# Performance work log

Measured on AMD Instinct MI355X. Metric: run time of the kernel, lower is better.

## Reference

```python
import jax, jax.numpy as jnp
import numpy as np

B, S, D = 2, 2048, 2048
NH, NKV = 32, 8
HD = D // NH           # 64
GS = NH // NKV         # 4
ROPE_BASE = 10000.0


def _rope_tables(seq_len, head_dim, base):
    inv_freq = 1.0 / (base ** (jnp.arange(head_dim // 2, dtype=jnp.float32) / (head_dim // 2)))
    angles = jnp.arange(seq_len, dtype=jnp.float32)[:, None] * inv_freq[None, :]  # [S, HD/2]
    angles = jnp.concatenate([angles, angles], axis=-1)                            # [S, HD]
    return jnp.cos(angles), jnp.sin(angles)


def _apply_rope(x, cos, sin):
    # x: [B, H, S, HD]
    hd = x.shape[-1]
    x1, x2 = x[..., : hd // 2], x[..., hd // 2 :]
    rotated = jnp.concatenate([-x2, x1], axis=-1)
    return (x * cos[None, None] + rotated * sin[None, None]).astype(x.dtype)


def setup_inputs() -> dict:
    key = jax.random.key(0)
    ks = jax.random.split(key, 5)
    scale = 0.02
    return {
        "x": jax.random.normal(ks[0], (B, S, D), dtype=jnp.float32),
        "Wq": jax.random.normal(ks[1], (D, D), dtype=jnp.float32) * scale,
        "Wk": jax.random.normal(ks[2], (D, NKV * HD), dtype=jnp.float32) * scale,
        "Wv": jax.random.normal(ks[3], (D, NKV * HD), dtype=jnp.float32) * scale,
        "Wo": jax.random.normal(ks[4], (D, D), dtype=jnp.float32) * scale,
    }


def reference(x, Wq, Wk, Wv, Wo):
    b, n, _ = x.shape
    cos, sin = _rope_tables(n, HD, ROPE_BASE)

    q = (x @ Wq).reshape(b, n, NH, HD).transpose(0, 2, 1, 3)    # [B, NH, S, HD]
    k = (x @ Wk).reshape(b, n, NKV, HD).transpose(0, 2, 1, 3)   # [B, NKV, S, HD]
    v = (x @ Wv).reshape(b, n, NKV, HD).transpose(0, 2, 1, 3)

    q = _apply_rope(q, cos, sin)
    k = _apply_rope(k, cos, sin)

    # GQA head sharing: repeat_interleave KV groups to full head count
    k = jnp.repeat(k, GS, axis=1)   # [B, NH, S, HD]
    v = jnp.repeat(v, GS, axis=1)

    scores = jnp.einsum("bhqd,bhkd->bhqk", q, k)                # [B, NH, S, S]
    causal = jnp.triu(jnp.ones((n, n), dtype=bool), k=1)
    scores = jnp.where(causal[None, None], -jnp.inf, scores)
    weights = jax.nn.softmax(scores / jnp.sqrt(jnp.float32(HD)), axis=-1)

    ctx = jnp.einsum("bhqk,bhkd->bhqd", weights, v)             # [B, NH, S, HD]
    ctx = ctx.transpose(0, 2, 1, 3).reshape(b, n, D)
    return ctx @ Wo
```

## Files before the change

### kernel.cpp

```cpp
#include <hip/hip_runtime.h>

typedef __bf16 bf16;
typedef __attribute__((ext_vector_type(8))) __bf16 bf16x8;
typedef __attribute__((ext_vector_type(4))) float f32x4;
typedef __attribute__((ext_vector_type(4))) short s16x4;

#define S_LEN 2048
#define D_MODEL 2048
#define NHEADS 32
#define NKVH 8
#define HDIM 64
#define BATCH 2

__device__ __forceinline__ void async_cp16(const bf16* g, bf16* l) {
    __builtin_amdgcn_global_load_lds(
        (const __attribute__((address_space(1))) unsigned int*)g,
        (__attribute__((address_space(3))) unsigned int*)l, 16, 0, 0);
}

__global__ void cvt_f32_bf16(const float* __restrict__ in, bf16* __restrict__ out, int n4) {
    int i = blockIdx.x * blockDim.x + threadIdx.x;
    if (i < n4) {
        float4 f = ((const float4*)in)[i];
        union { bf16 h[4]; uint2 u; } t;
        t.h[0] = (bf16)f.x; t.h[1] = (bf16)f.y; t.h[2] = (bf16)f.z; t.h[3] = (bf16)f.w;
        ((uint2*)out)[i] = t.u;
    }
}

__global__ void transpose_w(const float* __restrict__ W, bf16* __restrict__ Wt, int K, int N) {
    __shared__ float tile[32][33];
    int kt = blockIdx.y * 32, nt = blockIdx.x * 32;
    int tx = threadIdx.x, ty = threadIdx.y;
    #pragma unroll
    for (int i = 0; i < 32; i += 8)
        tile[ty + i][tx] = W[(size_t)(kt + ty + i) * N + nt + tx];
    __syncthreads();
    #pragma unroll
    for (int i = 0; i < 32; i += 8)
        Wt[(size_t)(nt + ty + i) * K + kt + tx] = (bf16)tile[tx][ty + i];
}

__global__ void transpose_v(const bf16* __restrict__ QKV, bf16* __restrict__ Vt) {
    __shared__ bf16 tl[32][33];
    int z = blockIdx.z;
    int s0 = blockIdx.x * 32, d0 = blockIdx.y * 32;
    int bb = z >> 3, hh = z & 7;
    int tx = threadIdx.x, ty = threadIdx.y;
    #pragma unroll
    for (int i = 0; i < 32; i += 8)
        tl[ty + i][tx] = QKV[((size_t)(bb * S_LEN + s0 + ty + i)) * 3072 + 2560 + hh * 64 + d0 + tx];
    __syncthreads();
    #pragma unroll
    for (int i = 0; i < 32; i += 8)
        Vt[((size_t)z * 64 + d0 + ty + i) * S_LEN + s0 + tx] = tl[tx][ty + i];
}

template <bool OUT_BF16>
__global__ __launch_bounds__(256) void gemm_bt(const bf16* __restrict__ A,
                                               const bf16* __restrict__ Bt,
                                               void* __restrict__ Cv,
                                               int M, int N, int K) {
    __shared__ __align__(16) bf16 As[128 * 64];
    __shared__ __align__(16) bf16 Bs[128 * 64];

    const int tid  = threadIdx.x;
    const int wave = tid >> 6;
    const int lane = tid & 63;
    const int l16  = lane & 15;
    const int quad = lane >> 4;
    const int wrow = (wave >> 1) * 64;
    const int wcol = (wave & 1) * 64;
    const int m0 = blockIdx.y * 128;
    const int n0 = blockIdx.x * 128;

    const int krow = lane >> 3;
    const int kc   = (lane & 7) ^ krow;
    const bf16* gA = A  + (size_t)(m0 + wave * 32 + krow) * K + kc * 8;
    const bf16* gB = Bt + (size_t)(n0 + wave * 32 + krow) * K + kc * 8;
    bf16* lA = &As[wave * 2048];
    bf16* lB = &Bs[wave * 2048];
    const size_t rstep = (size_t)8 * K;

    const int sw = l16 & 7;

    f32x4 acc[4][4];
    #pragma unroll
    for (int mi = 0; mi < 4; ++mi)
        #pragma unroll
        for (int ni = 0; ni < 4; ++ni)
            acc[mi][ni] = (f32x4){0.f, 0.f, 0.f, 0.f};

    for (int k0 = 0; k0 < K; k0 += 64) {
        __syncthreads();
        async_cp16(gA,             lA);
        async_cp16(gA +     rstep, lA + 512);
        async_cp16(gA + 2 * rstep, lA + 1024);
        async_cp16(gA + 3 * rstep, lA + 1536);
        async_cp16(gB,             lB);
        async_cp16(gB +     rstep, lB + 512);
        async_cp16(gB + 2 * rstep, lB + 1024);
        async_cp16(gB + 3 * rstep, lB + 1536);
        gA += 64; gB += 64;
        __syncthreads();

        #pragma unroll
        for (int kk = 0; kk < 2; ++kk) {
            bf16x8 af[4], bfr[4];
            #pragma unroll
            for (int mi = 0; mi < 4; ++mi)
                af[mi] = *(const bf16x8*)&As[(wrow + mi * 16 + l16) * 64 + (((kk * 4 + quad) ^ sw) * 8)];
            #pragma unroll
            for (int ni = 0; ni < 4; ++ni)
                bfr[ni] = *(const bf16x8*)&Bs[(wcol + ni * 16 + l16) * 64 + (((kk * 4 + quad) ^ sw) * 8)];
            #pragma unroll
            for (int mi = 0; mi < 4; ++mi)
                #pragma unroll
                for (int ni = 0; ni < 4; ++ni)
                    acc[mi][ni] = __builtin_amdgcn_mfma_f32_16x16x32_bf16(af[mi], bfr[ni], acc[mi][ni], 0, 0, 0);
        }
    }

    #pragma unroll
    for (int mi = 0; mi < 4; ++mi) {
        #pragma unroll
        for (int ni = 0; ni < 4; ++ni) {
            #pragma unroll
            for (int r = 0; r < 4; ++r) {
                size_t row = (size_t)(m0 + wrow + mi * 16 + quad * 4 + r);
                size_t col = (size_t)(n0 + wcol + ni * 16 + l16);
                if (OUT_BF16) ((bf16*)Cv)[row * N + col] = (bf16)acc[mi][ni][r];
                else          ((float*)Cv)[row * N + col] = acc[mi][ni][r];
            }
        }
    }
}

__global__ void rope_relayout(const bf16* __restrict__ QKV,
                              bf16* __restrict__ Qr, bf16* __restrict__ Kr) {
    const int QN = BATCH * S_LEN * NHEADS * 32;
    const int KN = BATCH * S_LEN * NKVH * 32;
    const float LC = 0.28782313662425572f;
    int idx = blockIdx.x * 256 + threadIdx.x;
    if (idx < QN) {
        int j = idx & 31, hh = (idx >> 5) & 31, s = (idx >> 10) & 2047, bb = idx >> 21;
        size_t src = ((size_t)(bb * S_LEN + s)) * 3072 + hh * HDIM + j;
        float x1 = (float)QKV[src], x2 = (float)QKV[src + 32];
        float ang = (float)s * __expf(-(float)j * LC);
        float sn, cs; sincosf(ang, &sn, &cs);
        size_t dst = ((size_t)((bb * NHEADS + hh) * S_LEN + s)) * HDIM + j;
        Qr[dst]      = (bf16)((x1 * cs - x2 * sn) * 0.125f);
        Qr[dst + 32] = (bf16)((x2 * cs + x1 * sn) * 0.125f);
    } else if (idx < QN + KN) {
        int t = idx - QN;
        int j = t & 31, hh = (t >> 5) & 7, s = (t >> 8) & 2047, bb = t >> 19;
        size_t src = ((size_t)(bb * S_LEN + s)) * 3072 + 2048 + hh * HDIM + j;
        float x1 = (float)QKV[src], x2 = (float)QKV[src + 32];
        float ang = (float)s * __expf(-(float)j * LC);
        float sn, cs; sincosf(ang, &sn, &cs);
        size_t dst = ((size_t)((bb * NKVH + hh) * S_LEN + s)) * HDIM + j;
        Kr[dst]      = (bf16)(x1 * cs - x2 * sn);
        Kr[dst + 32] = (bf16)(x2 * cs + x1 * sn);
    }
}

__global__ __launch_bounds__(256, 3) void attn_kernel(const bf16* __restrict__ Q,
                                                      const bf16* __restrict__ K,
                                                      const bf16* __restrict__ Vt,
                                                      bf16* __restrict__ Ctx) {
    __shared__ __align__(16) bf16 KsL[128 * 64];
    __shared__ __align__(16) bf16 VtL[64 * 128];

    static const signed char QTAB[16] = {15,14,13,12, 10,11,8,9, 5,4,7,6, 0,1,2,3};
    const int bx = blockIdx.x;
    const int qt = QTAB[((bx >> 8) << 2) | ((bx >> 6) & 3)];
    const int bh = bx & 63;
    const int b  = bh >> 5;
    const int h  = bh & 31;
    const int kvh = h >> 2;
    const int tid = threadIdx.x;
    const int wave = tid >> 6;
    const int lane = tid & 63;
    const int l16  = lane & 15;
    const int quad = lane >> 4;

    const bf16* Qb = Q  + ((size_t)(b * NHEADS + h)) * S_LEN * HDIM;
    const bf16* Kb = K  + ((size_t)(b * NKVH + kvh)) * S_LEN * HDIM;
    const bf16* Vb = Vt + ((size_t)(b * NKVH + kvh)) * HDIM * S_LEN;

    const int q0 = qt * 128;

    bf16x8 aq[2][2];
    #pragma unroll
    for (int qf = 0; qf < 2; ++qf)
        #pragma unroll
        for (int ks = 0; ks < 2; ++ks)
            aq[qf][ks] = *(const bf16x8*)(Qb + (size_t)(q0 + wave * 32 + qf * 16 + l16) * HDIM + ks * 32 + quad * 8);

    f32x4 O[2][4];
    float M0 = -1e30f, M1 = -1e30f;
    float l0 = 0.f, l1 = 0.f;
    #pragma unroll
    for (int qf = 0; qf < 2; ++qf)
        #pragma unroll
        for (int df = 0; df < 4; ++df) O[qf][df] = (f32x4){0.f,0.f,0.f,0.f};

    const int krow = lane >> 3, kslot = lane & 7;
    const int kc   = kslot ^ (krow & 7);
    const int vslot = lane & 15, vsub = lane >> 4;

    #pragma unroll 1
    for (int kt = 0; kt <= qt; ++kt) {
        const int k0 = kt * 128;
        __syncthreads();
        #pragma unroll
        for (int j = 0; j < 4; ++j) {
            int rbase = (wave * 4 + j) * 8;
            async_cp16(Kb + (size_t)(k0 + rbase + krow) * HDIM + kc * 8, &KsL[rbase * 64]);
            int d0 = (wave * 4 + j) * 4;
            int vrow = d0 + vsub;
            int vc = vslot ^ (vrow & 15);
            async_cp16(Vb + (size_t)vrow * S_LEN + k0 + vc * 8, &VtL[d0 * 128]);
        }
        __syncthreads();

        f32x4 sc[2][8];
        #pragma unroll
        for (int kf = 0; kf < 8; ++kf) {
            sc[0][kf] = (f32x4){0.f,0.f,0.f,0.f};
            sc[1][kf] = (f32x4){0.f,0.f,0.f,0.f};
            #pragma unroll
            for (int ks = 0; ks < 2; ++ks) {
                bf16x8 bk = *(const bf16x8*)&KsL[(kf * 16 + l16) * 64 + (((ks * 4 + quad) ^ (l16 & 7)) * 8)];
                sc[0][kf] = __builtin_amdgcn_mfma_f32_16x16x32_bf16(bk, aq[0][ks], sc[0][kf], 0, 0, 0);
                sc[1][kf] = __builtin_amdgcn_mfma_f32_16x16x32_bf16(bk, aq[1][ks], sc[1][kf], 0, 0, 0);
            }
        }

        if (kt == qt) {
            #pragma unroll
            for (int kf = 0; kf < 8; ++kf)
                #pragma unroll
                for (int r = 0; r < 4; ++r) {
                    int key = kf * 16 + quad * 4 + r;
                    int qi0 = wave * 32 + l16;
                    if (key > qi0)      sc[0][kf][r] = -1e30f;
                    if (key > qi0 + 16) sc[1][kf][r] = -1e30f;
                }
        }

        float mx0 = sc[0][0][0], mx1 = sc[1][0][0];
        #pragma unroll
        for (int kf = 0; kf < 8; ++kf)
            #pragma unroll
            for (int r = 0; r < 4; ++r) {
                mx0 = fmaxf(mx0, sc[0][kf][r]);
                mx1 = fmaxf(mx1, sc[1][kf][r]);
            }
        mx0 = fmaxf(mx0, __shfl_xor(mx0, 16)); mx0 = fmaxf(mx0, __shfl_xor(mx0, 32));
        mx1 = fmaxf(mx1, __shfl_xor(mx1, 16)); mx1 = fmaxf(mx1, __shfl_xor(mx1, 32));

        float Mn0 = fmaxf(M0, mx0), Mn1 = fmaxf(M1, mx1);
        float a0 = __expf(M0 - Mn0), a1 = __expf(M1 - Mn1);
        M0 = Mn0; M1 = Mn1;
        l0 *= a0; l1 *= a1;

        #pragma unroll
        for (int r = 0; r < 4; ++r) {
            float aO0 = __shfl(a0, quad * 4 + r);
            float aO1 = __shfl(a1, quad * 4 + r);
            #pragma unroll
            for (int df = 0; df < 4; ++df) {
                O[0][df][r] *= aO0;
                O[1][df][r] *= aO1;
            }
        }

        #pragma unroll
        for (int kf = 0; kf < 8; ++kf)
            #pragma unroll
            for (int r = 0; r < 4; ++r) {
                float e0 = __expf(sc[0][kf][r] - M0); sc[0][kf][r] = e0; l0 += e0;
                float e1 = __expf(sc[1][kf][r] - M1); sc[1][kf][r] = e1; l1 += e1;
            }

        #pragma unroll
        for (int kf = 0; kf < 8; ++kf) {
            union { bf16 hh[4]; s16x4 s4; } p0, p1;
            #pragma unroll
            for (int r = 0; r < 4; ++r) {
                p0.hh[r] = (bf16)sc[0][kf][r];
                p1.hh[r] = (bf16)sc[1][kf][r];
            }
            #pragma unroll
            for (int df = 0; df < 4; ++df) {
                s16x4 bv = *(const s16x4*)&VtL[(df * 16 + l16) * 128 +
                                               (((kf * 2 + (quad >> 1)) ^ l16) * 8) + (quad & 1) * 4];
                O[0][df] = __builtin_amdgcn_mfma_f32_16x16x16bf16_1k(p0.s4, bv, O[0][df], 0, 0, 0);
                O[1][df] = __builtin_amdgcn_mfma_f32_16x16x16bf16_1k(p1.s4, bv, O[1][df], 0, 0, 0);
            }
        }
    }

    l0 += __shfl_xor(l0, 16); l0 += __shfl_xor(l0, 32);
    l1 += __shfl_xor(l1, 16); l1 += __shfl_xor(l1, 32);
    #pragma unroll
    for (int r = 0; r < 4; ++r) {
        float inv0 = 1.0f / __shfl(l0, quad * 4 + r);
        float inv1 = 1.0f / __shfl(l1, quad * 4 + r);
        size_t row0 = (size_t)b * S_LEN + q0 + wave * 32 + quad * 4 + r;
        bf16* dst0 = Ctx + row0 * D_MODEL + h * HDIM;
        bf16* dst1 = dst0 + (size_t)16 * D_MODEL;
        #pragma unroll
        for (int df = 0; df < 4; ++df) {
            dst0[df * 16 + l16] = (bf16)(O[0][df][r] * inv0);
            dst1[df * 16 + l16] = (bf16)(O[1][df][r] * inv1);
        }
    }
}

extern "C" void kernel_launch(void* const* d_in, const int* in_sizes, int n_in,
                              void* d_out, int out_size, void* d_ws, size_t ws_size,
                              hipStream_t stream) {
    const float* x  = (const float*)d_in[0];
    const float* Wq = (const float*)d_in[1];
    const float* Wk = (const float*)d_in[2];
    const float* Wv = (const float*)d_in[3];
    const float* Wo = (const float*)d_in[4];

    char* p = (char*)d_ws;
    bf16* X16 = (bf16*)p; p += (size_t)4096 * 2048 * 2;
    bf16* WqT = (bf16*)p; p += (size_t)2048 * 2048 * 2;
    bf16* WkT = (bf16*)p; p += (size_t)512 * 2048 * 2;
    bf16* WvT = (bf16*)p; p += (size_t)512 * 2048 * 2;
    bf16* WoT = (bf16*)p; p += (size_t)2048 * 2048 * 2;
    bf16* QKV = (bf16*)p; p += (size_t)4096 * 3072 * 2;
    bf16* Qr  = (bf16*)p; p += (size_t)4096 * 2048 * 2;
    bf16* Kr  = (bf16*)p; p += (size_t)4096 * 512 * 2;
    bf16* Vt  = (bf16*)p; p += (size_t)16 * 64 * 2048 * 2;
    bf16* Ctx = QKV;

    cvt_f32_bf16<<<8192, 256, 0, stream>>>(x, X16, 2097152);
    transpose_w<<<dim3(64, 64), dim3(32, 8), 0, stream>>>(Wq, WqT, 2048, 2048);
    transpose_w<<<dim3(16, 64), dim3(32, 8), 0, stream>>>(Wk, WkT, 2048, 512);
    transpose_w<<<dim3(16, 64), dim3(32, 8), 0, stream>>>(Wv, WvT, 2048, 512);
    transpose_w<<<dim3(64, 64), dim3(32, 8), 0, stream>>>(Wo, WoT, 2048, 2048);

    gemm_bt<true><<<dim3(24, 32), 256, 0, stream>>>(X16, WqT, (void*)QKV, 4096, 3072, 2048);

    rope_relayout<<<20480, 256, 0, stream>>>(QKV, Qr, Kr);
    transpose_v<<<dim3(64, 2, 16), dim3(32, 8), 0, stream>>>(QKV, Vt);
    attn_kernel<<<1024, 256, 0, stream>>>(Qr, Kr, Vt, Ctx);

    gemm_bt<false><<<dim3(16, 32), 256, 0, stream>>>(Ctx, WoT, d_out, 4096, 2048, 2048);
}
```

Before: 299.8 us.

## Merge prep kernels and streamline attention softmax with exp2 and lazy rescale

Folds the x conversion and the four weight transposes into one preprocessing launch, and merges RoPE with the V transpose, cutting the launch count. In attention, the log2e factor is folded into the Q scale so exp2 replaces expf. The running max and output rescale are updated only when some row's max grows by more than a threshold. Row sums are accumulated with an MFMA against a ones vector instead of scalar adds and shuffles, and launch bounds are raised to four blocks per CU. The lazy rescale trades a wave-wide vote for skipped rescales, and the higher occupancy target may force register spills.

```diff
diff --git a/kernel.cpp b/kernel.cpp
--- a/kernel.cpp
+++ b/kernel.cpp
@@ -18,20 +18,31 @@
         (__attribute__((address_space(3))) unsigned int*)l, 16, 0, 0);
 }
 
-__global__ void cvt_f32_bf16(const float* __restrict__ in, bf16* __restrict__ out, int n4) {
-    int i = blockIdx.x * blockDim.x + threadIdx.x;
-    if (i < n4) {
-        float4 f = ((const float4*)in)[i];
+__global__ void preproc(const float* __restrict__ x,
+                        const float* __restrict__ Wq, const float* __restrict__ Wk,
+                        const float* __restrict__ Wv, const float* __restrict__ Wo,
+                        bf16* __restrict__ X16, bf16* __restrict__ WqT, bf16* __restrict__ WkT,
+                        bf16* __restrict__ WvT, bf16* __restrict__ WoT) {
+    __shared__ float tile[32][33];
+    const int tid = threadIdx.x;
+    int bid = blockIdx.x;
+    if (bid < 8192) {
+        int i = bid * 256 + tid;
+        float4 f = ((const float4*)x)[i];
         union { bf16 h[4]; uint2 u; } t;
         t.h[0] = (bf16)f.x; t.h[1] = (bf16)f.y; t.h[2] = (bf16)f.z; t.h[3] = (bf16)f.w;
-        ((uint2*)out)[i] = t.u;
-    }
-}
-
-__global__ void transpose_w(const float* __restrict__ W, bf16* __restrict__ Wt, int K, int N) {
-    __shared__ float tile[32][33];
-    int kt = blockIdx.y * 32, nt = blockIdx.x * 32;
-    int tx = threadIdx.x, ty = threadIdx.y;
+        ((uint2*)X16)[i] = t.u;
+        return;
+    }
+    int l = bid - 8192;
+    const float* W; bf16* Wt; int N, bx, by;
+    const int K = 2048;
+    if (l < 4096)      {            W = Wq; Wt = WqT; N = 2048; bx = l & 63; by = l >> 6; }
+    else if (l < 5120) { l -= 4096; W = Wk; Wt = WkT; N = 512;  bx = l & 15; by = l >> 4; }
+    else if (l < 6144) { l -= 5120; W = Wv; Wt = WvT; N = 512;  bx = l & 15; by = l >> 4; }
+    else               { l -= 6144; W = Wo; Wt = WoT; N = 2048; bx = l & 63; by = l >> 6; }
+    const int kt = by * 32, nt = bx * 32;
+    const int tx = tid & 31, ty = tid >> 5;
     #pragma unroll
     for (int i = 0; i < 32; i += 8)
         tile[ty + i][tx] = W[(size_t)(kt + ty + i) * N + nt + tx];
@@ -39,21 +50,6 @@
     #pragma unroll
     for (int i = 0; i < 32; i += 8)
         Wt[(size_t)(nt + ty + i) * K + kt + tx] = (bf16)tile[tx][ty + i];
-}
-
-__global__ void transpose_v(const bf16* __restrict__ QKV, bf16* __restrict__ Vt) {
-    __shared__ bf16 tl[32][33];
-    int z = blockIdx.z;
-    int s0 = blockIdx.x * 32, d0 = blockIdx.y * 32;
-    int bb = z >> 3, hh = z & 7;
-    int tx = threadIdx.x, ty = threadIdx.y;
-    #pragma unroll
-    for (int i = 0; i < 32; i += 8)
-        tl[ty + i][tx] = QKV[((size_t)(bb * S_LEN + s0 + ty + i)) * 3072 + 2560 + hh * 64 + d0 + tx];
-    __syncthreads();
-    #pragma unroll
-    for (int i = 0; i < 32; i += 8)
-        Vt[((size_t)z * 64 + d0 + ty + i) * S_LEN + s0 + tx] = tl[tx][ty + i];
 }
 
 template <bool OUT_BF16>
@@ -136,35 +132,55 @@
     }
 }
 
-__global__ void rope_relayout(const bf16* __restrict__ QKV,
-                              bf16* __restrict__ Qr, bf16* __restrict__ Kr) {
-    const int QN = BATCH * S_LEN * NHEADS * 32;
-    const int KN = BATCH * S_LEN * NKVH * 32;
+__global__ void rope_tv(const bf16* __restrict__ QKV,
+                        bf16* __restrict__ Qr, bf16* __restrict__ Kr,
+                        bf16* __restrict__ Vt) {
+    __shared__ bf16 tl[32][33];
+    const int tid = threadIdx.x;
+    const int bid = blockIdx.x;
     const float LC = 0.28782313662425572f;
-    int idx = blockIdx.x * 256 + threadIdx.x;
-    if (idx < QN) {
-        int j = idx & 31, hh = (idx >> 5) & 31, s = (idx >> 10) & 2047, bb = idx >> 21;
-        size_t src = ((size_t)(bb * S_LEN + s)) * 3072 + hh * HDIM + j;
-        float x1 = (float)QKV[src], x2 = (float)QKV[src + 32];
-        float ang = (float)s * __expf(-(float)j * LC);
-        float sn, cs; sincosf(ang, &sn, &cs);
-        size_t dst = ((size_t)((bb * NHEADS + hh) * S_LEN + s)) * HDIM + j;
-        Qr[dst]      = (bf16)((x1 * cs - x2 * sn) * 0.125f);
-        Qr[dst + 32] = (bf16)((x2 * cs + x1 * sn) * 0.125f);
-    } else if (idx < QN + KN) {
-        int t = idx - QN;
-        int j = t & 31, hh = (t >> 5) & 7, s = (t >> 8) & 2047, bb = t >> 19;
-        size_t src = ((size_t)(bb * S_LEN + s)) * 3072 + 2048 + hh * HDIM + j;
-        float x1 = (float)QKV[src], x2 = (float)QKV[src + 32];
-        float ang = (float)s * __expf(-(float)j * LC);
-        float sn, cs; sincosf(ang, &sn, &cs);
-        size_t dst = ((size_t)((bb * NKVH + hh) * S_LEN + s)) * HDIM + j;
-        Kr[dst]      = (bf16)(x1 * cs - x2 * sn);
-        Kr[dst + 32] = (bf16)(x2 * cs + x1 * sn);
-    }
-}
-
-__global__ __launch_bounds__(256, 3) void attn_kernel(const bf16* __restrict__ Q,
+    const float QS = 0.18033688011112042f;
+    if (bid < 20480) {
+        const int QN = BATCH * S_LEN * NHEADS * 32;
+        int idx = bid * 256 + tid;
+        if (idx < QN) {
+            int j = idx & 31, hh = (idx >> 5) & 31, s = (idx >> 10) & 2047, bb = idx >> 21;
+            size_t src = ((size_t)(bb * S_LEN + s)) * 3072 + hh * HDIM + j;
+            float x1 = (float)QKV[src], x2 = (float)QKV[src + 32];
+            float ang = (float)s * __expf(-(float)j * LC);
+            float sn, cs; sincosf(ang, &sn, &cs);
+            size_t dst = ((size_t)((bb * NHEADS + hh) * S_LEN + s)) * HDIM + j;
+            Qr[dst]      = (bf16)((x1 * cs - x2 * sn) * QS);
+            Qr[dst + 32] = (bf16)((x2 * cs + x1 * sn) * QS);
+        } else {
+            int t = idx - QN;
+            int j = t & 31, hh = (t >> 5) & 7, s = (t >> 8) & 2047, bb = t >> 19;
+            size_t src = ((size_t)(bb * S_LEN + s)) * 3072 + 2048 + hh * HDIM + j;
+            float x1 = (float)QKV[src], x2 = (float)QKV[src + 32];
+            float ang = (float)s * __expf(-(float)j * LC);
+            float sn, cs; sincosf(ang, &sn, &cs);
+            size_t dst = ((size_t)((bb * NKVH + hh) * S_LEN + s)) * HDIM + j;
+            Kr[dst]      = (bf16)(x1 * cs - x2 * sn);
+            Kr[dst + 32] = (bf16)(x2 * cs + x1 * sn);
+        }
+        return;
+    }
+    int l = bid - 20480;
+    int s0 = (l & 63) * 32;
+    int d0 = ((l >> 6) & 1) * 32;
+    int z  = l >> 7;
+    int bb = z >> 3, hh = z & 7;
+    int tx = tid & 31, ty = tid >> 5;
+    #pragma unroll
+    for (int i = 0; i < 32; i += 8)
+        tl[ty + i][tx] = QKV[((size_t)(bb * S_LEN + s0 + ty + i)) * 3072 + 2560 + hh * 64 + d0 + tx];
+    __syncthreads();
+    #pragma unroll
+    for (int i = 0; i < 32; i += 8)
+        Vt[((size_t)z * 64 + d0 + ty + i) * S_LEN + s0 + tx] = tl[tx][ty + i];
+}
+
+__global__ __launch_bounds__(256, 4) void attn_kernel(const bf16* __restrict__ Q,
                                                       const bf16* __restrict__ K,
                                                       const bf16* __restrict__ Vt,
                                                       bf16* __restrict__ Ctx) {
@@ -198,12 +214,15 @@
             aq[qf][ks] = *(const bf16x8*)(Qb + (size_t)(q0 + wave * 32 + qf * 16 + l16) * HDIM + ks * 32 + quad * 8);
 
     f32x4 O[2][4];
+    f32x4 lacc0 = (f32x4){0.f,0.f,0.f,0.f};
+    f32x4 lacc1 = (f32x4){0.f,0.f,0.f,0.f};
     float M0 = -1e30f, M1 = -1e30f;
-    float l0 = 0.f, l1 = 0.f;
     #pragma unroll
     for (int qf = 0; qf < 2; ++qf)
         #pragma unroll
         for (int df = 0; df < 4; ++df) O[qf][df] = (f32x4){0.f,0.f,0.f,0.f};
+
+    const s16x4 ones = (s16x4){(short)0x3F80, (short)0x3F80, (short)0x3F80, (short)0x3F80};
 
     const int krow = lane >> 3, kslot = lane & 7;
     const int kc   = kslot ^ (krow & 7);
@@ -249,30 +268,33 @@
                 }
         }
 
-        float mx0 = sc[0][0][0], mx1 = sc[1][0][0];
-        #pragma unroll
-        for (int kf = 0; kf < 8; ++kf)
-            #pragma unroll
-            for (int r = 0; r < 4; ++r) {
-                mx0 = fmaxf(mx0, sc[0][kf][r]);
-                mx1 = fmaxf(mx1, sc[1][kf][r]);
-            }
+        float mx0 = -1e30f, mx1 = -1e30f;
+        #pragma unroll
+        for (int kf = 0; kf < 8; ++kf) {
+            float t0 = fmaxf(fmaxf(sc[0][kf][0], sc[0][kf][1]), fmaxf(sc[0][kf][2], sc[0][kf][3]));
+            float t1 = fmaxf(fmaxf(sc[1][kf][0], sc[1][kf][1]), fmaxf(sc[1][kf][2], sc[1][kf][3]));
+            mx0 = fmaxf(mx0, t0);
+            mx1 = fmaxf(mx1, t1);
+        }
         mx0 = fmaxf(mx0, __shfl_xor(mx0, 16)); mx0 = fmaxf(mx0, __shfl_xor(mx0, 32));
         mx1 = fmaxf(mx1, __shfl_xor(mx1, 16)); mx1 = fmaxf(mx1, __shfl_xor(mx1, 32));
 
-        float Mn0 = fmaxf(M0, mx0), Mn1 = fmaxf(M1, mx1);
-        float a0 = __expf(M0 - Mn0), a1 = __expf(M1 - Mn1);
-        M0 = Mn0; M1 = Mn1;
-        l0 *= a0; l1 *= a1;
-
-        #pragma unroll
-        for (int r = 0; r < 4; ++r) {
-            float aO0 = __shfl(a0, quad * 4 + r);
-            float aO1 = __shfl(a1, quad * 4 + r);
-            #pragma unroll
-            for (int df = 0; df < 4; ++df) {
-                O[0][df][r] *= aO0;
-                O[1][df][r] *= aO1;
+        if (!__all((mx0 <= M0 + 8.0f) && (mx1 <= M1 + 8.0f))) {
+            float Mn0 = fmaxf(M0, mx0), Mn1 = fmaxf(M1, mx1);
+            float a0 = __builtin_amdgcn_exp2f(M0 - Mn0);
+            float a1 = __builtin_amdgcn_exp2f(M1 - Mn1);
+            M0 = Mn0; M1 = Mn1;
+            #pragma unroll
+            for (int r = 0; r < 4; ++r) {
+                float aO0 = __shfl(a0, quad * 4 + r);
+                float aO1 = __shfl(a1, quad * 4 + r);
+                lacc0[r] *= aO0;
+                lacc1[r] *= aO1;
+                #pragma unroll
+                for (int df = 0; df < 4; ++df) {
+                    O[0][df][r] *= aO0;
+                    O[1][df][r] *= aO1;
+                }
             }
         }
 
@@ -280,8 +302,8 @@
         for (int kf = 0; kf < 8; ++kf)
             #pragma unroll
             for (int r = 0; r < 4; ++r) {
-                float e0 = __expf(sc[0][kf][r] - M0); sc[0][kf][r] = e0; l0 += e0;
-                float e1 = __expf(sc[1][kf][r] - M1); sc[1][kf][r] = e1; l1 += e1;
+                sc[0][kf][r] = __builtin_amdgcn_exp2f(sc[0][kf][r] - M0);
+                sc[1][kf][r] = __builtin_amdgcn_exp2f(sc[1][kf][r] - M1);
             }
 
         #pragma unroll
@@ -292,6 +314,8 @@
                 p0.hh[r] = (bf16)sc[0][kf][r];
                 p1.hh[r] = (bf16)sc[1][kf][r];
             }
+            lacc0 = __builtin_amdgcn_mfma_f32_16x16x16bf16_1k(p0.s4, ones, lacc0, 0, 0, 0);
+            lacc1 = __builtin_amdgcn_mfma_f32_16x16x16bf16_1k(p1.s4, ones, lacc1, 0, 0, 0);
             #pragma unroll
             for (int df = 0; df < 4; ++df) {
                 s16x4 bv = *(const s16x4*)&VtL[(df * 16 + l16) * 128 +
@@ -302,12 +326,10 @@
         }
     }
 
-    l0 += __shfl_xor(l0, 16); l0 += __shfl_xor(l0, 32);
-    l1 += __shfl_xor(l1, 16); l1 += __shfl_xor(l1, 32);
     #pragma unroll
     for (int r = 0; r < 4; ++r) {
-        float inv0 = 1.0f / __shfl(l0, quad * 4 + r);
-        float inv1 = 1.0f / __shfl(l1, quad * 4 + r);
+        float inv0 = 1.0f / lacc0[r];
+        float inv1 = 1.0f / lacc1[r];
         size_t row0 = (size_t)b * S_LEN + q0 + wave * 32 + quad * 4 + r;
         bf16* dst0 = Ctx + row0 * D_MODEL + h * HDIM;
         bf16* dst1 = dst0 + (size_t)16 * D_MODEL;
@@ -340,16 +362,12 @@
     bf16* Vt  = (bf16*)p; p += (size_t)16 * 64 * 2048 * 2;
     bf16* Ctx = QKV;
 
-    cvt_f32_bf16<<<8192, 256, 0, stream>>>(x, X16, 2097152);
-    transpose_w<<<dim3(64, 64), dim3(32, 8), 0, stream>>>(Wq, WqT, 2048, 2048);
-    transpose_w<<<dim3(16, 64), dim3(32, 8), 0, stream>>>(Wk, WkT, 2048, 512);
-    transpose_w<<<dim3(16, 64), dim3(32, 8), 0, stream>>>(Wv, WvT, 2048, 512);
-    transpose_w<<<dim3(64, 64), dim3(32, 8), 0, stream>>>(Wo, WoT, 2048, 2048);
+    preproc<<<18432, 256, 0, stream>>>(x, Wq, Wk, Wv, Wo, X16, WqT, WkT, WvT, WoT);
 
     gemm_bt<true><<<dim3(24, 32), 256, 0, stream>>>(X16, WqT, (void*)QKV, 4096, 3072, 2048);
 
-    rope_relayout<<<20480, 256, 0, stream>>>(QKV, Qr, Kr);
-    transpose_v<<<dim3(64, 2, 16), dim3(32, 8), 0, stream>>>(QKV, Vt);
+    rope_tv<<<22528, 256, 0, stream>>>(QKV, Qr, Kr, Vt);
+
     attn_kernel<<<1024, 256, 0, stream>>>(Qr, Kr, Vt, Ctx);
 
     gemm_bt<false><<<dim3(16, 32), 256, 0, stream>>>(Ctx, WoT, d_out, 4096, 2048, 2048);
```

After: 374.4 us. 1.25x slower.
